# Performance work log

Hardware: AMD Instinct MI355X
Metric: run time of the kernel (lower is better)

The kernel has to match this reference:

```python
import jax, jax.numpy as jnp
import numpy as np

WIN = 7          # window_size (square)
N = WIN * WIN    # tokens per window = 49
C = 384          # channels
H = 12           # heads
HD = C // H      # head dim = 32
NW = 4           # shifted-window mask groups
BW = 4096        # total windows (batch*num_windows)
SCALE = HD ** -0.5


def _relative_position_index():
    coords_h = np.arange(WIN)
    coords_w = np.arange(WIN)
    coords = np.stack(np.meshgrid(coords_h, coords_w, indexing='ij'))  # [2,7,7]
    cf = coords.reshape(2, -1)                                         # [2,49]
    rel = cf[:, :, None] - cf[:, None, :]                              # [2,49,49]
    rel = rel.transpose(1, 2, 0)
    rel[:, :, 0] += WIN - 1
    rel[:, :, 1] += WIN - 1
    rel[:, :, 0] *= 2 * WIN - 1
    return rel.sum(-1).astype(np.int32)                                # [49,49]


def setup_inputs() -> dict:
    key = jax.random.key(0)
    ks = jax.random.split(key, 7)
    x = jax.random.normal(ks[0], (BW, N, C), dtype=jnp.float32)
    mask = jax.random.normal(ks[1], (NW, N, N), dtype=jnp.float32)
    w_qkv = jax.random.normal(ks[2], (C, 3 * C), dtype=jnp.float32) * 0.02
    b_qkv = jnp.zeros((3 * C,), dtype=jnp.float32)
    bias_table = jax.random.normal(ks[3], ((2 * WIN - 1) ** 2, H), dtype=jnp.float32) * 0.02
    w_proj = jax.random.normal(ks[4], (C, C), dtype=jnp.float32) * 0.02
    b_proj = jnp.zeros((C,), dtype=jnp.float32)
    rel_index = jnp.asarray(_relative_position_index())
    return {"x": x, "mask": mask, "w_qkv": w_qkv, "b_qkv": b_qkv,
            "bias_table": bias_table, "w_proj": w_proj, "b_proj": b_proj,
            "rel_index": rel_index}


def reference(x, mask, w_qkv, b_qkv, bias_table, w_proj, b_proj, rel_index):
    B = x.shape[0]
    # QKV projection: [B,N,3C] -> [3,B,H,N,hd]
    qkv = x @ w_qkv + b_qkv
    qkv = qkv.reshape(B, N, 3, H, HD).transpose(2, 0, 3, 1, 4)
    q, k, v = qkv[0], qkv[1], qkv[2]
    q = q * SCALE
    attn = jnp.einsum('bhnd,bhmd->bhnm', q, k)          # [B,H,N,N]
    # gathered relative position bias: [N,N,H] -> [H,N,N]
    bias = bias_table[rel_index]                         # [N,N,H]
    attn = attn + bias.transpose(2, 0, 1)[None]
    # shift-window mask add
    attn = attn.reshape(B // NW, NW, H, N, N) + mask[None, :, None]
    attn = attn.reshape(B, H, N, N)
    attn = jax.nn.softmax(attn, axis=-1)
    out = jnp.einsum('bhnm,bhmd->bhnd', attn, v)         # [B,H,N,hd]
    out = out.transpose(0, 2, 1, 3).reshape(B, N, C)
    out = out @ w_proj + b_proj
    return out
```

## Files before the change

kernel.cpp:

```cpp
#include <hip/hip_runtime.h>

typedef unsigned short u16;
typedef u16 u16x4 __attribute__((ext_vector_type(4)));
typedef u16 u16x8 __attribute__((ext_vector_type(8)));
typedef __bf16 bf16x8 __attribute__((ext_vector_type(8)));
typedef float f32x4 __attribute__((ext_vector_type(4)));

#define MFMA16 __builtin_amdgcn_mfma_f32_16x16x32_bf16
#define QSCALE 0.17677669529663689f
#define VMWAIT(N) asm volatile("s_waitcnt vmcnt(" #N ")" ::: "memory")

__device__ __forceinline__ u16 f2bf(float f) {
  unsigned u = __builtin_bit_cast(unsigned, f);
  u += 0x7fffu + ((u >> 16) & 1u);
  return (u16)(u >> 16);
}
__device__ __forceinline__ bf16x8 as_bf(u16x8 u) { return __builtin_bit_cast(bf16x8, u); }
__device__ __forceinline__ f32x4 zf4() { f32x4 z = {0.f, 0.f, 0.f, 0.f}; return z; }

template <int CTRL>
__device__ __forceinline__ float dppf(float x) {
  int i = __builtin_bit_cast(int, x);
  int r = __builtin_amdgcn_update_dpp(i, i, CTRL, 0xf, 0xf, false);
  return __builtin_bit_cast(float, r);
}
__device__ __forceinline__ float rmax16(float x) {
  x = fmaxf(x, dppf<0xB1>(x));
  x = fmaxf(x, dppf<0x4E>(x));
  x = fmaxf(x, dppf<0x124>(x));
  x = fmaxf(x, dppf<0x128>(x));
  return x;
}
__device__ __forceinline__ float rsum16(float x) {
  x += dppf<0xB1>(x);
  x += dppf<0x4E>(x);
  x += dppf<0x124>(x);
  x += dppf<0x128>(x);
  return x;
}

__global__ __launch_bounds__(256) void prep_kernel(
    const float* __restrict__ wq, const float* __restrict__ wp,
    const float* __restrict__ bt, const int* __restrict__ ri,
    const float* __restrict__ mask,
    u16* __restrict__ wqT, u16* __restrict__ wpT, float* __restrict__ smask2) {
  int idx = blockIdx.x * 256 + threadIdx.x;
  if (idx < 442368) {
    int nn = idx / 384, kk = idx % 384;
    wqT[idx] = f2bf(wq[(size_t)kk * 1152 + nn]);
  } else if (idx < 589824) {
    int i2 = idx - 442368;
    int nn = i2 / 384, kk = i2 % 384;
    wpT[i2] = f2bf(wp[(size_t)kk * 384 + nn]);
  } else if (idx < 740352) {
    int i3 = idx - 589824;
    int g = i3 / 37632;
    int rem = i3 % 37632;
    int h = rem / 3136;
    int nm = rem % 3136;
    int n = nm >> 6;
    int r2 = nm & 63;
    int lane = r2 >> 2, nj = r2 & 3;
    int m = nj * 16 + lane;
    float v = 0.f;
    if (m < 49 && n < 49)
      v = bt[ri[n * 49 + m] * 12 + h] + mask[g * 2401 + n * 49 + m];
    smask2[i3] = v;
  }
}

__global__ __launch_bounds__(256) void conv_x(const float* __restrict__ x,
                                              u16* __restrict__ xb) {
  size_t i = ((size_t)blockIdx.x * 256 + threadIdx.x) * 8;
  f32x4 a = *(const f32x4*)(x + i);
  f32x4 b = *(const f32x4*)(x + i + 4);
  u16x8 o;
  o[0] = f2bf(a[0]); o[1] = f2bf(a[1]); o[2] = f2bf(a[2]); o[3] = f2bf(a[3]);
  o[4] = f2bf(b[0]); o[5] = f2bf(b[1]); o[6] = f2bf(b[2]); o[7] = f2bf(b[3]);
  *(u16x8*)(xb + i) = o;
}

__global__ __launch_bounds__(512) void gemm_qkv8(
    const u16* __restrict__ Wt, const u16* __restrict__ Xb,
    const float* __restrict__ bias, u16* __restrict__ outp) {
  __shared__ u16 As[2][128 * 32];
  __shared__ u16 Bs[2][256 * 32];
  const int t = threadIdx.x;
  const int l = t & 63, w = t >> 6;

  const int bid = blockIdx.x;
  const int xcd = bid & 7, q = bid >> 3;
  const int logical = xcd * 882 + q;
  const int tokt = logical / 9, cht = logical % 9;
  const int tb = tokt * 256;
  const int cb = cht * 128;

  f32x4 acc[4][4];
#pragma unroll
  for (int mi = 0; mi < 4; ++mi)
#pragma unroll
    for (int ni = 0; ni < 4; ++ni) acc[mi][ni] = zf4();

  const int rA = (w >> 2) * 64 + (l & 15);
  const int rB = (w & 3) * 64 + (l & 15);
  const int gsel = l >> 4;
  const int gA = ((gsel ^ ((rA >> 1) & 3))) * 8;
  const int gB = ((gsel ^ ((rB >> 1) & 3))) * 8;

  auto stage = [&](int bf, int kt) {
    const int ko = kt * 32;
    {
      const int row = t >> 2, slot = t & 3;
      const int sg = (slot ^ ((row >> 1) & 3)) * 8;
      __builtin_amdgcn_global_load_lds(
          (const __attribute__((address_space(1))) unsigned int*)
              (Wt + (size_t)(cb + row) * 384 + ko + sg),
          (__attribute__((address_space(3))) unsigned int*)(&As[bf][t * 8]),
          16, 0, 0);
    }
#pragma unroll
    for (int j = 0; j < 2; ++j) {
      const int gi = j * 512 + t;
      const int row = gi >> 2, slot = gi & 3;
      const int sg = (slot ^ ((row >> 1) & 3)) * 8;
      __builtin_amdgcn_global_load_lds(
          (const __attribute__((address_space(1))) unsigned int*)
              (Xb + (size_t)(tb + row) * 384 + ko + sg),
          (__attribute__((address_space(3))) unsigned int*)(&Bs[bf][gi * 8]),
          16, 0, 0);
    }
  };

  auto kbody = [&](int cur, int ktnext, bool dostage) {
    __builtin_amdgcn_sched_barrier(0);
    __builtin_amdgcn_s_barrier();
    bf16x8 af[4], bfr[4];
#pragma unroll
    for (int mi = 0; mi < 4; ++mi)
      af[mi] = *(const bf16x8*)(&As[cur][(rA + mi * 16) * 32 + gA]);
#pragma unroll
    for (int nj = 0; nj < 4; ++nj)
      bfr[nj] = *(const bf16x8*)(&Bs[cur][(rB + nj * 16) * 32 + gB]);
    asm volatile("s_waitcnt lgkmcnt(0)" ::: "memory");
    __builtin_amdgcn_sched_barrier(0);
    __builtin_amdgcn_s_barrier();
    if (dostage) stage(cur, ktnext);
    __builtin_amdgcn_sched_barrier(0);
    __builtin_amdgcn_s_setprio(1);
#pragma unroll
    for (int mi = 0; mi < 4; ++mi)
#pragma unroll
      for (int nj = 0; nj < 4; ++nj)
        acc[mi][nj] = MFMA16(af[mi], bfr[nj], acc[mi][nj], 0, 0, 0);
    __builtin_amdgcn_s_setprio(0);
  };

  stage(0, 0);
  stage(1, 1);
#pragma unroll
  for (int kt = 0; kt < 10; ++kt) {
    VMWAIT(3);
    kbody(kt & 1, kt + 2, true);
  }
  VMWAIT(3);
  kbody(0, 0, false);
  VMWAIT(0);
  kbody(1, 0, false);

#pragma unroll
  for (int mi = 0; mi < 4; ++mi) {
    const int ch = cb + (w >> 2) * 64 + mi * 16 + (l >> 4) * 4;
    const f32x4 bv = *(const f32x4*)(bias + ch);
    const int qkvi = ch / 384;
    const int rem = ch - qkvi * 384;
    const int hh = rem >> 5;
    const int d = rem & 31;
    const float scl = (qkvi == 0) ? QSCALE : 1.0f;
#pragma unroll
    for (int nj = 0; nj < 4; ++nj) {
      const int tok = tb + (w & 3) * 64 + nj * 16 + (l & 15);
      u16x4 pk;
#pragma unroll
      for (int r = 0; r < 4; ++r) pk[r] = f2bf((acc[mi][nj][r] + bv[r]) * scl);
      *(u16x4*)(outp + ((size_t)(qkvi * 12 + hh) * 200704 + tok) * 32 + d) = pk;
    }
  }
}

__global__ __launch_bounds__(256) void gemm_proj(
    const u16* __restrict__ Wt, const u16* __restrict__ Xb,
    const float* __restrict__ bias, float* __restrict__ outp) {
  __shared__ u16 As[2][128 * 32];
  __shared__ u16 Bs[2][128 * 32];
  const int t = threadIdx.x;
  const int l = t & 63, w = t >> 6;

  const int bid = blockIdx.x;
  const int xcd = bid & 7, q = bid >> 3;
  const int logical = xcd * (196 * 3) + q;
  const int tokt = logical / 3, cht = logical % 3;
  const int tb = tokt * 128;
  const int cb = cht * 128;

  f32x4 acc[4][4];
#pragma unroll
  for (int mi = 0; mi < 4; ++mi)
#pragma unroll
    for (int ni = 0; ni < 4; ++ni) acc[mi][ni] = zf4();

  const int rA = (w >> 1) * 64 + (l & 15);
  const int rB = (w & 1) * 64 + (l & 15);
  const int gsel = l >> 4;
  const int gA = ((gsel ^ ((rA >> 1) & 3))) * 8;
  const int gB = ((gsel ^ ((rB >> 1) & 3))) * 8;

  auto stage = [&](int bf, int kt) {
    const int ko = kt * 32;
#pragma unroll
    for (int j = 0; j < 2; ++j) {
      const int gi = j * 256 + t;
      const int row = gi >> 2, slot = gi & 3;
      const int sg = (slot ^ ((row >> 1) & 3)) * 8;
      __builtin_amdgcn_global_load_lds(
          (const __attribute__((address_space(1))) unsigned int*)
              (Wt + (size_t)(cb + row) * 384 + ko + sg),
          (__attribute__((address_space(3))) unsigned int*)(&As[bf][gi * 8]),
          16, 0, 0);
      __builtin_amdgcn_global_load_lds(
          (const __attribute__((address_space(1))) unsigned int*)
              (Xb + (size_t)(tb + row) * 384 + ko + sg),
          (__attribute__((address_space(3))) unsigned int*)(&Bs[bf][gi * 8]),
          16, 0, 0);
    }
  };

  auto kbody = [&](int cur, int ktnext, bool dostage) {
    __builtin_amdgcn_sched_barrier(0);
    __builtin_amdgcn_s_barrier();
    bf16x8 af[4], bfr[4];
#pragma unroll
    for (int mi = 0; mi < 4; ++mi)
      af[mi] = *(const bf16x8*)(&As[cur][(rA + mi * 16) * 32 + gA]);
#pragma unroll
    for (int nj = 0; nj < 4; ++nj)
      bfr[nj] = *(const bf16x8*)(&Bs[cur][(rB + nj * 16) * 32 + gB]);
    asm volatile("s_waitcnt lgkmcnt(0)" ::: "memory");
    __builtin_amdgcn_sched_barrier(0);
    __builtin_amdgcn_s_barrier();
    if (dostage) stage(cur, ktnext);
    __builtin_amdgcn_sched_barrier(0);
    __builtin_amdgcn_s_setprio(1);
#pragma unroll
    for (int mi = 0; mi < 4; ++mi)
#pragma unroll
      for (int nj = 0; nj < 4; ++nj)
        acc[mi][nj] = MFMA16(af[mi], bfr[nj], acc[mi][nj], 0, 0, 0);
    __builtin_amdgcn_s_setprio(0);
  };

  stage(0, 0);
  stage(1, 1);
#pragma unroll
  for (int kt = 0; kt < 10; ++kt) {
    VMWAIT(4);
    kbody(kt & 1, kt + 2, true);
  }
  VMWAIT(4);
  kbody(0, 0, false);
  VMWAIT(0);
  kbody(1, 0, false);

#pragma unroll
  for (int mi = 0; mi < 4; ++mi) {
    const int ch = cb + (w >> 1) * 64 + mi * 16 + (l >> 4) * 4;
    const f32x4 bv = *(const f32x4*)(bias + ch);
#pragma unroll
    for (int nj = 0; nj < 4; ++nj) {
      const int tok = tb + (w & 1) * 64 + nj * 16 + (l & 15);
      f32x4 o;
#pragma unroll
      for (int r = 0; r < 4; ++r) o[r] = acc[mi][nj][r] + bv[r];
      *(f32x4*)(outp + (size_t)tok * 384 + ch) = o;
    }
  }
}

__global__ __launch_bounds__(256) void attn_kernel(
    const u16* __restrict__ qkvb, const float* __restrict__ smask2,
    u16* __restrict__ attnb) {
  __shared__ u16 Pl[4][4096];
  __shared__ u16 Vt[4][2336];
  const int t = threadIdx.x;
  const int l = t & 63, wv = t >> 6;
  const int bid = blockIdx.x;
  const int logical = (bid & 7) * 1536 + (bid >> 3);
  const int b = logical / 3;
  const int hg = logical % 3;
  const int h = hg * 4 + wv;
  u16* Pw = &Pl[wv][0];
  u16* Vw = &Vt[wv][0];
  const u16x8 z = {0, 0, 0, 0, 0, 0, 0, 0};

#pragma unroll
  for (int i = 0; i < 4; ++i) {
    const int row = i * 16 + (l >> 2);
    const int sg = l & 3;
    u16x8 vv = z;
    if (row < 49)
      vv = *(const u16x8*)(qkvb + ((size_t)(24 + h) * 200704 + b * 49 + row) * 32 + sg * 8);
#pragma unroll
    for (int e = 0; e < 8; ++e) {
      const int d = sg * 8 + e;
      Vw[d * 72 + (d >> 3) * 8 + row] = vv[e];
    }
  }

  const u16* qb = qkvb + ((size_t)h * 200704 + b * 49) * 32 + (l >> 4) * 8;
  const u16* kp = qkvb + ((size_t)(12 + h) * 200704 + b * 49) * 32 + (l >> 4) * 8;
  bf16x8 qa[4], kb[4];
#pragma unroll
  for (int mi = 0; mi < 4; ++mi) {
    const int n = mi * 16 + (l & 15);
    qa[mi] = (n < 49) ? *(const bf16x8*)(qb + n * 32) : as_bf(z);
    kb[mi] = (n < 49) ? *(const bf16x8*)(kp + n * 32) : as_bf(z);
  }

  f32x4 s[4][4];
  __builtin_amdgcn_s_setprio(1);
#pragma unroll
  for (int mi = 0; mi < 4; ++mi)
#pragma unroll
    for (int nj = 0; nj < 4; ++nj) s[mi][nj] = MFMA16(qa[mi], kb[nj], zf4(), 0, 0, 0);
  __builtin_amdgcn_s_setprio(0);

  const float* sm2 = smask2 + ((size_t)(b & 3) * 12 + h) * 3136;
#pragma unroll
  for (int mi = 0; mi < 4; ++mi) {
#pragma unroll
    for (int r = 0; r < 4; ++r) {
      const int n = mi * 16 + (l >> 4) * 4 + r;
      if (n < 49) {
        const f32x4 bv = *(const f32x4*)(sm2 + n * 64 + (l & 15) * 4);
        s[mi][0][r] += bv[0];
        s[mi][1][r] += bv[1];
        s[mi][2][r] += bv[2];
        s[mi][3][r] = ((l & 15) == 0) ? s[mi][3][r] + bv[3] : -1e30f;
      }
    }
  }
#pragma unroll
  for (int mi = 0; mi < 4; ++mi) {
#pragma unroll
    for (int r = 0; r < 4; ++r) {
      float mx = fmaxf(fmaxf(s[mi][0][r], s[mi][1][r]), fmaxf(s[mi][2][r], s[mi][3][r]));
      mx = rmax16(mx);
      float e0 = 0.f;
#pragma unroll
      for (int nj = 0; nj < 4; ++nj) {
        const float p = __expf(s[mi][nj][r] - mx);
        s[mi][nj][r] = p;
        e0 += p;
      }
      e0 = rsum16(e0);
      const float inv = 1.0f / e0;
#pragma unroll
      for (int nj = 0; nj < 4; ++nj) s[mi][nj][r] *= inv;
    }
  }
#pragma unroll
  for (int mi = 0; mi < 4; ++mi)
#pragma unroll
    for (int r = 0; r < 4; ++r) {
      const int row = mi * 16 + (l >> 4) * 4 + r;
#pragma unroll
      for (int nj = 0; nj < 4; ++nj) {
        const int col = nj * 16 + (l & 15);
        Pw[row * 64 + (((col >> 3) ^ (row & 7)) * 8) + (col & 7)] = f2bf(s[mi][nj][r]);
      }
    }
  asm volatile("s_waitcnt lgkmcnt(0)" ::: "memory");
  __builtin_amdgcn_sched_barrier(0);

  f32x4 ot[2][4];
#pragma unroll
  for (int dj = 0; dj < 2; ++dj)
#pragma unroll
    for (int mi = 0; mi < 4; ++mi) ot[dj][mi] = zf4();
#pragma unroll
  for (int ks = 0; ks < 2; ++ks) {
    bf16x8 va[2], pb[4];
#pragma unroll
    for (int dj = 0; dj < 2; ++dj) {
      const int d0 = dj * 16 + (l & 15);
      va[dj] = *(const bf16x8*)(Vw + d0 * 72 + (d0 >> 3) * 8 + ks * 32 + (l >> 4) * 8);
    }
#pragma unroll
    for (int mi = 0; mi < 4; ++mi) {
      const int row = mi * 16 + (l & 15);
      pb[mi] = *(const bf16x8*)(Pw + row * 64 + (((ks * 4 + (l >> 4)) ^ (l & 7)) * 8));
    }
    __builtin_amdgcn_s_setprio(1);
#pragma unroll
    for (int dj = 0; dj < 2; ++dj)
#pragma unroll
      for (int mi = 0; mi < 4; ++mi)
        ot[dj][mi] = MFMA16(va[dj], pb[mi], ot[dj][mi], 0, 0, 0);
    __builtin_amdgcn_s_setprio(0);
  }
#pragma unroll
  for (int dj = 0; dj < 2; ++dj)
#pragma unroll
    for (int mi = 0; mi < 4; ++mi) {
      const int n = mi * 16 + (l & 15);
      if (n < 49) {
        u16x4 pk;
        pk[0] = f2bf(ot[dj][mi][0]);
        pk[1] = f2bf(ot[dj][mi][1]);
        pk[2] = f2bf(ot[dj][mi][2]);
        pk[3] = f2bf(ot[dj][mi][3]);
        *(u16x4*)(attnb + (size_t)(b * 49 + n) * 384 + h * 32 + dj * 16 + (l >> 4) * 4) = pk;
      }
    }
}

extern "C" void kernel_launch(void* const* d_in, const int* in_sizes, int n_in,
                              void* d_out, int out_size, void* d_ws, size_t ws_size,
                              hipStream_t stream) {
  const float* x       = (const float*)d_in[0];
  const float* mask    = (const float*)d_in[1];
  const float* w_qkv   = (const float*)d_in[2];
  const float* b_qkv   = (const float*)d_in[3];
  const float* bias_t  = (const float*)d_in[4];
  const float* w_proj  = (const float*)d_in[5];
  const float* b_proj  = (const float*)d_in[6];
  const int*   rel_idx = (const int*)d_in[7];
  float* out = (float*)d_out;

  char* ws = (char*)d_ws;
  u16*   wqT    = (u16*)ws;
  u16*   wpT    = (u16*)(ws + 884736);
  float* smask2 = (float*)(ws + 1179648);
  u16*   qkvb   = (u16*)(ws + 1781760);
  u16*   xb     = (u16*)(ws + 464203776);
  u16*   attnb  = (u16*)(ws + 464203776);

  prep_kernel<<<2892, 256, 0, stream>>>(w_qkv, w_proj, bias_t, rel_idx, mask,
                                        wqT, wpT, smask2);
  conv_x<<<37632, 256, 0, stream>>>(x, xb);
  gemm_qkv8<<<7056, 512, 0, stream>>>(wqT, xb, b_qkv, qkvb);
  attn_kernel<<<12288, 256, 0, stream>>>(qkvb, smask2, attnb);
  gemm_proj<<<4704, 256, 0, stream>>>(wpT, attnb, b_proj, out);
}
```

Measured before the change: 812.9 us.

## Write V transposed per window from QKV GEMM and drop LDS V transpose in attention

The QKV GEMM now writes the V section directly into a per-head, per-window transposed layout (d-major, padded to 56 tokens), so the attention kernel can load V fragments straight from global memory instead of staging and transposing V through LDS. The QKV GEMM is also switched from the 512-thread 128x256 tile variant to the 256-thread 128x128 tile GEMM with twice as many blocks. The transposed V stores are scattered 2-byte writes, which may be costly, and padding columns 49..55 are never written, so they depend on workspace contents (the attention MFMA reads k up to 63, crossing into the next d row).

```diff
diff --git a/kernel.cpp b/kernel.cpp
--- a/kernel.cpp
+++ b/kernel.cpp
@@ -9,6 +9,9 @@
 #define MFMA16 __builtin_amdgcn_mfma_f32_16x16x32_bf16
 #define QSCALE 0.17677669529663689f
 #define VMWAIT(N) asm volatile("s_waitcnt vmcnt(" #N ")" ::: "memory")
+
+#define VT_OFF 154140672ull
+#define VT_TILE 1792
 
 __device__ __forceinline__ u16 f2bf(float f) {
   unsigned u = __builtin_bit_cast(unsigned, f);
@@ -80,116 +83,9 @@
   *(u16x8*)(xb + i) = o;
 }
 
-__global__ __launch_bounds__(512) void gemm_qkv8(
+__global__ __launch_bounds__(256) void gemm_qkv(
     const u16* __restrict__ Wt, const u16* __restrict__ Xb,
     const float* __restrict__ bias, u16* __restrict__ outp) {
-  __shared__ u16 As[2][128 * 32];
-  __shared__ u16 Bs[2][256 * 32];
-  const int t = threadIdx.x;
-  const int l = t & 63, w = t >> 6;
-
-  const int bid = blockIdx.x;
-  const int xcd = bid & 7, q = bid >> 3;
-  const int logical = xcd * 882 + q;
-  const int tokt = logical / 9, cht = logical % 9;
-  const int tb = tokt * 256;
-  const int cb = cht * 128;
-
-  f32x4 acc[4][4];
-#pragma unroll
-  for (int mi = 0; mi < 4; ++mi)
-#pragma unroll
-    for (int ni = 0; ni < 4; ++ni) acc[mi][ni] = zf4();
-
-  const int rA = (w >> 2) * 64 + (l & 15);
-  const int rB = (w & 3) * 64 + (l & 15);
-  const int gsel = l >> 4;
-  const int gA = ((gsel ^ ((rA >> 1) & 3))) * 8;
-  const int gB = ((gsel ^ ((rB >> 1) & 3))) * 8;
-
-  auto stage = [&](int bf, int kt) {
-    const int ko = kt * 32;
-    {
-      const int row = t >> 2, slot = t & 3;
-      const int sg = (slot ^ ((row >> 1) & 3)) * 8;
-      __builtin_amdgcn_global_load_lds(
-          (const __attribute__((address_space(1))) unsigned int*)
-              (Wt + (size_t)(cb + row) * 384 + ko + sg),
-          (__attribute__((address_space(3))) unsigned int*)(&As[bf][t * 8]),
-          16, 0, 0);
-    }
-#pragma unroll
-    for (int j = 0; j < 2; ++j) {
-      const int gi = j * 512 + t;
-      const int row = gi >> 2, slot = gi & 3;
-      const int sg = (slot ^ ((row >> 1) & 3)) * 8;
-      __builtin_amdgcn_global_load_lds(
-          (const __attribute__((address_space(1))) unsigned int*)
-              (Xb + (size_t)(tb + row) * 384 + ko + sg),
-          (__attribute__((address_space(3))) unsigned int*)(&Bs[bf][gi * 8]),
-          16, 0, 0);
-    }
-  };
-
-  auto kbody = [&](int cur, int ktnext, bool dostage) {
-    __builtin_amdgcn_sched_barrier(0);
-    __builtin_amdgcn_s_barrier();
-    bf16x8 af[4], bfr[4];
-#pragma unroll
-    for (int mi = 0; mi < 4; ++mi)
-      af[mi] = *(const bf16x8*)(&As[cur][(rA + mi * 16) * 32 + gA]);
-#pragma unroll
-    for (int nj = 0; nj < 4; ++nj)
-      bfr[nj] = *(const bf16x8*)(&Bs[cur][(rB + nj * 16) * 32 + gB]);
-    asm volatile("s_waitcnt lgkmcnt(0)" ::: "memory");
-    __builtin_amdgcn_sched_barrier(0);
-    __builtin_amdgcn_s_barrier();
-    if (dostage) stage(cur, ktnext);
-    __builtin_amdgcn_sched_barrier(0);
-    __builtin_amdgcn_s_setprio(1);
-#pragma unroll
-    for (int mi = 0; mi < 4; ++mi)
-#pragma unroll
-      for (int nj = 0; nj < 4; ++nj)
-        acc[mi][nj] = MFMA16(af[mi], bfr[nj], acc[mi][nj], 0, 0, 0);
-    __builtin_amdgcn_s_setprio(0);
-  };
-
-  stage(0, 0);
-  stage(1, 1);
-#pragma unroll
-  for (int kt = 0; kt < 10; ++kt) {
-    VMWAIT(3);
-    kbody(kt & 1, kt + 2, true);
-  }
-  VMWAIT(3);
-  kbody(0, 0, false);
-  VMWAIT(0);
-  kbody(1, 0, false);
-
-#pragma unroll
-  for (int mi = 0; mi < 4; ++mi) {
-    const int ch = cb + (w >> 2) * 64 + mi * 16 + (l >> 4) * 4;
-    const f32x4 bv = *(const f32x4*)(bias + ch);
-    const int qkvi = ch / 384;
-    const int rem = ch - qkvi * 384;
-    const int hh = rem >> 5;
-    const int d = rem & 31;
-    const float scl = (qkvi == 0) ? QSCALE : 1.0f;
-#pragma unroll
-    for (int nj = 0; nj < 4; ++nj) {
-      const int tok = tb + (w & 3) * 64 + nj * 16 + (l & 15);
-      u16x4 pk;
-#pragma unroll
-      for (int r = 0; r < 4; ++r) pk[r] = f2bf((acc[mi][nj][r] + bv[r]) * scl);
-      *(u16x4*)(outp + ((size_t)(qkvi * 12 + hh) * 200704 + tok) * 32 + d) = pk;
-    }
-  }
-}
-
-__global__ __launch_bounds__(256) void gemm_proj(
-    const u16* __restrict__ Wt, const u16* __restrict__ Xb,
-    const float* __restrict__ bias, float* __restrict__ outp) {
   __shared__ u16 As[2][128 * 32];
   __shared__ u16 Bs[2][128 * 32];
   const int t = threadIdx.x;
@@ -197,8 +93,8 @@
 
   const int bid = blockIdx.x;
   const int xcd = bid & 7, q = bid >> 3;
-  const int logical = xcd * (196 * 3) + q;
-  const int tokt = logical / 3, cht = logical % 3;
+  const int logical = xcd * (196 * 9) + q;
+  const int tokt = logical / 9, cht = logical % 9;
   const int tb = tokt * 128;
   const int cb = cht * 128;
 
@@ -274,6 +170,118 @@
   for (int mi = 0; mi < 4; ++mi) {
     const int ch = cb + (w >> 1) * 64 + mi * 16 + (l >> 4) * 4;
     const f32x4 bv = *(const f32x4*)(bias + ch);
+    const int qkvi = ch / 384;
+    const int rem = ch - qkvi * 384;
+    const int hh = rem >> 5;
+    const int d = rem & 31;
+    const float scl = (qkvi == 0) ? QSCALE : 1.0f;
+#pragma unroll
+    for (int nj = 0; nj < 4; ++nj) {
+      const int tok = tb + (w & 1) * 64 + nj * 16 + (l & 15);
+      u16x4 pk;
+#pragma unroll
+      for (int r = 0; r < 4; ++r) pk[r] = f2bf((acc[mi][nj][r] + bv[r]) * scl);
+      if (qkvi < 2) {
+        *(u16x4*)(outp + ((size_t)(qkvi * 12 + hh) * 200704 + tok) * 32 + d) = pk;
+      } else {
+        const int w0 = tok / 49;
+        const int k0 = tok - w0 * 49;
+        u16* vt = outp + VT_OFF;
+#pragma unroll
+        for (int r = 0; r < 4; ++r)
+          vt[(size_t)(hh * 4096 + w0) * VT_TILE + (d + r) * 56 + k0] = pk[r];
+      }
+    }
+  }
+}
+
+__global__ __launch_bounds__(256) void gemm_proj(
+    const u16* __restrict__ Wt, const u16* __restrict__ Xb,
+    const float* __restrict__ bias, float* __restrict__ outp) {
+  __shared__ u16 As[2][128 * 32];
+  __shared__ u16 Bs[2][128 * 32];
+  const int t = threadIdx.x;
+  const int l = t & 63, w = t >> 6;
+
+  const int bid = blockIdx.x;
+  const int xcd = bid & 7, q = bid >> 3;
+  const int logical = xcd * (196 * 3) + q;
+  const int tokt = logical / 3, cht = logical % 3;
+  const int tb = tokt * 128;
+  const int cb = cht * 128;
+
+  f32x4 acc[4][4];
+#pragma unroll
+  for (int mi = 0; mi < 4; ++mi)
+#pragma unroll
+    for (int ni = 0; ni < 4; ++ni) acc[mi][ni] = zf4();
+
+  const int rA = (w >> 1) * 64 + (l & 15);
+  const int rB = (w & 1) * 64 + (l & 15);
+  const int gsel = l >> 4;
+  const int gA = ((gsel ^ ((rA >> 1) & 3))) * 8;
+  const int gB = ((gsel ^ ((rB >> 1) & 3))) * 8;
+
+  auto stage = [&](int bf, int kt) {
+    const int ko = kt * 32;
+#pragma unroll
+    for (int j = 0; j < 2; ++j) {
+      const int gi = j * 256 + t;
+      const int row = gi >> 2, slot = gi & 3;
+      const int sg = (slot ^ ((row >> 1) & 3)) * 8;
+      __builtin_amdgcn_global_load_lds(
+          (const __attribute__((address_space(1))) unsigned int*)
+              (Wt + (size_t)(cb + row) * 384 + ko + sg),
+          (__attribute__((address_space(3))) unsigned int*)(&As[bf][gi * 8]),
+          16, 0, 0);
+      __builtin_amdgcn_global_load_lds(
+          (const __attribute__((address_space(1))) unsigned int*)
+              (Xb + (size_t)(tb + row) * 384 + ko + sg),
+          (__attribute__((address_space(3))) unsigned int*)(&Bs[bf][gi * 8]),
+          16, 0, 0);
+    }
+  };
+
+  auto kbody = [&](int cur, int ktnext, bool dostage) {
+    __builtin_amdgcn_sched_barrier(0);
+    __builtin_amdgcn_s_barrier();
+    bf16x8 af[4], bfr[4];
+#pragma unroll
+    for (int mi = 0; mi < 4; ++mi)
+      af[mi] = *(const bf16x8*)(&As[cur][(rA + mi * 16) * 32 + gA]);
+#pragma unroll
+    for (int nj = 0; nj < 4; ++nj)
+      bfr[nj] = *(const bf16x8*)(&Bs[cur][(rB + nj * 16) * 32 + gB]);
+    asm volatile("s_waitcnt lgkmcnt(0)" ::: "memory");
+    __builtin_amdgcn_sched_barrier(0);
+    __builtin_amdgcn_s_barrier();
+    if (dostage) stage(cur, ktnext);
+    __builtin_amdgcn_sched_barrier(0);
+    __builtin_amdgcn_s_setprio(1);
+#pragma unroll
+    for (int mi = 0; mi < 4; ++mi)
+#pragma unroll
+      for (int nj = 0; nj < 4; ++nj)
+        acc[mi][nj] = MFMA16(af[mi], bfr[nj], acc[mi][nj], 0, 0, 0);
+    __builtin_amdgcn_s_setprio(0);
+  };
+
+  stage(0, 0);
+  stage(1, 1);
+#pragma unroll
+  for (int kt = 0; kt < 10; ++kt) {
+    VMWAIT(4);
+    kbody(kt & 1, kt + 2, true);
+  }
+  VMWAIT(4);
+  kbody(0, 0, false);
+  VMWAIT(0);
+  kbody(1, 0, false);
+
+#pragma unroll
+  for (int mi = 0; mi < 4; ++mi) {
+    const int ch = cb + (w >> 1) * 64 + mi * 16 + (l >> 4) * 4;
+    const f32x4 bv = *(const f32x4*)(bias + ch);
 #pragma unroll
     for (int nj = 0; nj < 4; ++nj) {
       const int tok = tb + (w & 1) * 64 + nj * 16 + (l & 15);
@@ -289,7 +297,6 @@
     const u16* __restrict__ qkvb, const float* __restrict__ smask2,
     u16* __restrict__ attnb) {
   __shared__ u16 Pl[4][4096];
-  __shared__ u16 Vt[4][2336];
   const int t = threadIdx.x;
   const int l = t & 63, wv = t >> 6;
   const int bid = blockIdx.x;
@@ -298,22 +305,7 @@
   const int hg = logical % 3;
   const int h = hg * 4 + wv;
   u16* Pw = &Pl[wv][0];
-  u16* Vw = &Vt[wv][0];
   const u16x8 z = {0, 0, 0, 0, 0, 0, 0, 0};
-
-#pragma unroll
-  for (int i = 0; i < 4; ++i) {
-    const int row = i * 16 + (l >> 2);
-    const int sg = l & 3;
-    u16x8 vv = z;
-    if (row < 49)
-      vv = *(const u16x8*)(qkvb + ((size_t)(24 + h) * 200704 + b * 49 + row) * 32 + sg * 8);
-#pragma unroll
-    for (int e = 0; e < 8; ++e) {
-      const int d = sg * 8 + e;
-      Vw[d * 72 + (d >> 3) * 8 + row] = vv[e];
-    }
-  }
 
   const u16* qb = qkvb + ((size_t)h * 200704 + b * 49) * 32 + (l >> 4) * 8;
   const u16* kp = qkvb + ((size_t)(12 + h) * 200704 + b * 49) * 32 + (l >> 4) * 8;
@@ -381,6 +373,7 @@
   asm volatile("s_waitcnt lgkmcnt(0)" ::: "memory");
   __builtin_amdgcn_sched_barrier(0);
 
+  const u16* vtb = qkvb + VT_OFF + (size_t)(h * 4096 + b) * VT_TILE;
   f32x4 ot[2][4];
 #pragma unroll
   for (int dj = 0; dj < 2; ++dj)
@@ -392,7 +385,7 @@
 #pragma unroll
     for (int dj = 0; dj < 2; ++dj) {
       const int d0 = dj * 16 + (l & 15);
-      va[dj] = *(const bf16x8*)(Vw + d0 * 72 + (d0 >> 3) * 8 + ks * 32 + (l >> 4) * 8);
+      va[dj] = *(const bf16x8*)(vtb + d0 * 56 + ks * 32 + (l >> 4) * 8);
     }
 #pragma unroll
     for (int mi = 0; mi < 4; ++mi) {
@@ -441,13 +434,13 @@
   u16*   wpT    = (u16*)(ws + 884736);
   float* smask2 = (float*)(ws + 1179648);
   u16*   qkvb   = (u16*)(ws + 1781760);
-  u16*   xb     = (u16*)(ws + 464203776);
-  u16*   attnb  = (u16*)(ws + 464203776);
+  u16*   xb     = (u16*)(ws + 486223872);
+  u16*   attnb  = (u16*)(ws + 486223872);
 
   prep_kernel<<<2892, 256, 0, stream>>>(w_qkv, w_proj, bias_t, rel_idx, mask,
                                         wqT, wpT, smask2);
   conv_x<<<37632, 256, 0, stream>>>(x, xb);
-  gemm_qkv8<<<7056, 512, 0, stream>>>(wqT, xb, b_qkv, qkvb);
+  gemm_qkv<<<14112, 256, 0, stream>>>(wqT, xb, b_qkv, qkvb);
   attn_kernel<<<12288, 256, 0, stream>>>(qkvb, smask2, attnb);
   gemm_proj<<<4704, 256, 0, stream>>>(wpT, attnb, b_proj, out);
 }
```

New measurement: 750.0 us. 1.08x faster.
